# Kernel tuning notes

Measured on AMD Instinct MI355X. Metric: run time of the kernel, lower is better.

The kernel has to match this reference:

```python
import jax, jax.numpy as jnp
import numpy as np

N_Q = 8          # number of residual quantizer stages
N_CODES = 1024   # 2 ** (75 // N_q + 1)
D = 128
GAMMA = 0.99


def setup_inputs() -> dict:
    key = jax.random.key(0)
    k1, k2, k3, k4 = jax.random.split(key, 4)
    data_object = jax.random.normal(k1, (16, D, 2048), dtype=jnp.float32)
    weights = jax.random.normal(k2, (N_Q, N_CODES, D), dtype=jnp.float32)
    # EMA cluster-size buffer; scale so most codes are 'alive' (>= 2)
    N_i = jax.random.uniform(k3, (N_Q, N_CODES), dtype=jnp.float32) * 100.0
    m_i = jax.random.normal(k4, (N_Q, N_CODES, D), dtype=jnp.float32)
    return {"data_object": data_object, "weights": weights, "N_i": N_i, "m_i": m_i}


def reference(data_object, weights, N_i, m_i):
    b, d, s = data_object.shape
    y = jnp.transpose(data_object, (0, 2, 1))  # [b, s, D]
    residual = y
    cur_y = jnp.zeros_like(y)
    all_idx, new_Ni, new_mi, new_W = [], [], [], []
    key = jax.random.key(42)
    one_m_g = 1.0 - GAMMA
    for i in range(N_Q):
        W = weights[i]  # [N, D]
        # squared euclidean distances: ||y||^2 + ||W||^2 - 2 y.W^T  -> [b, s, N]
        dist = ((residual ** 2).sum(-1)[..., None]
                + (W ** 2).sum(-1)[None, None, :]
                - 2.0 * jnp.einsum('bsd,nd->bsn', residual, W))
        idx = jnp.argmin(dist, axis=-1)          # [b, s]
        Q = W[idx]                               # gather  [b, s, D]
        cur_y = cur_y + Q
        flat_idx = idx.reshape(-1)               # [b*s]
        flat_res = residual.reshape(-1, d)       # [b*s, D]
        # fused scatter-reduce replacing the torch per-code mask loop
        counts = jax.ops.segment_sum(jnp.ones(flat_idx.shape, jnp.float32),
                                     flat_idx, num_segments=N_CODES)
        sums = jax.ops.segment_sum(flat_res, flat_idx, num_segments=N_CODES)
        Ni_new = N_i[i] * GAMMA + counts * one_m_g
        mi_new = m_i[i] * GAMMA + sums * one_m_g
        w_new = mi_new / jnp.clip(Ni_new, 1e-8)[:, None]
        # dead-code replacement with random residual vectors
        dead = Ni_new < 2.0
        rid = jax.random.randint(jax.random.fold_in(key, i), (N_CODES,),
                                 0, flat_res.shape[0])
        w_new = jnp.where(dead[:, None], flat_res[rid], w_new)
        all_idx.append(idx)
        new_Ni.append(Ni_new)
        new_mi.append(mi_new)
        new_W.append(w_new)
        residual = residual - Q
    cur_y_t = jnp.transpose(cur_y, (0, 2, 1))  # [b, D, s]
    # straight-through estimator
    logits = data_object + jax.lax.stop_gradient(cur_y_t - data_object)
    commitment_loss = jnp.mean((jax.lax.stop_gradient(cur_y_t) - data_object) ** 2)
    indices = jnp.stack(all_idx, axis=0)  # [N_q, b, s]
    return (logits, commitment_loss, indices,
            jnp.stack(new_Ni), jnp.stack(new_mi), jnp.stack(new_W))
```

## Files before the change

### kernel.cpp

```cpp
#include <hip/hip_runtime.h>
#include <hip/hip_bf16.h>

#define NQ 8
#define NC 1024
#define DD 128
#define BB 16
#define SS 2048
#define RR (BB * SS)
#define GAMMA_F 0.99f
#define TAU 0.03f

typedef __attribute__((ext_vector_type(8))) short bf16x8;
typedef __attribute__((ext_vector_type(4))) float f32x4;

__device__ __forceinline__ ushort f2bf(float x) {
  __hip_bfloat16 b = __float2bfloat16(x);
  return *reinterpret_cast<ushort*>(&b);
}
__device__ __forceinline__ float bf2f(ushort u) {
  unsigned v = ((unsigned)u) << 16;
  return *reinterpret_cast<float*>(&v);
}

__global__ __launch_bounds__(256) void k_transpose_in(
    const float* __restrict__ data, float* __restrict__ res)
{
  __shared__ float tile[32][33];
  int b = blockIdx.z;
  int s0 = blockIdx.x << 5, d0 = blockIdx.y << 5;
  int tx = threadIdx.x, ty = threadIdx.y;
  #pragma unroll
  for (int r = 0; r < 32; r += 8)
    tile[ty + r][tx] = data[((size_t)b * DD + d0 + ty + r) * SS + s0 + tx];
  __syncthreads();
  #pragma unroll
  for (int r = 0; r < 32; r += 8)
    res[((size_t)b * SS + s0 + ty + r) * DD + d0 + tx] = tile[tx][ty + r];
}

__global__ void k_wsq(const float* __restrict__ W, float* __restrict__ wsq)
{
  int c = blockIdx.x * blockDim.x + threadIdx.x;
  if (c >= NQ * NC) return;
  const float4* p = reinterpret_cast<const float4*>(W + (size_t)c * DD);
  float s = 0.f;
  #pragma unroll 8
  for (int k = 0; k < DD / 4; ++k) {
    float4 v = p[k];
    s += v.x * v.x + v.y * v.y + v.z * v.z + v.w * v.w;
  }
  wsq[c] = s;
}

__global__ __launch_bounds__(256) void k_split(
    const float* __restrict__ src, ushort* __restrict__ dst)
{
  int i = blockIdx.x * 256 + threadIdx.x;
  int row = i >> 2, ks = i & 3;
  const float4* sp = reinterpret_cast<const float4*>(src + (size_t)row * DD + ks * 32);
  size_t gb = ((size_t)(row >> 4) * 8 + ks * 2) * 64 + (row & 15);
  #pragma unroll
  for (int kg = 0; kg < 4; ++kg) {
    float4 a = sp[kg * 2], b = sp[kg * 2 + 1];
    ushort4 h0, h1, l0, l1;
    h0.x = f2bf(a.x); l0.x = f2bf(a.x - bf2f(h0.x));
    h0.y = f2bf(a.y); l0.y = f2bf(a.y - bf2f(h0.y));
    h0.z = f2bf(a.z); l0.z = f2bf(a.z - bf2f(h0.z));
    h0.w = f2bf(a.w); l0.w = f2bf(a.w - bf2f(h0.w));
    h1.x = f2bf(b.x); l1.x = f2bf(b.x - bf2f(h1.x));
    h1.y = f2bf(b.y); l1.y = f2bf(b.y - bf2f(h1.y));
    h1.z = f2bf(b.z); l1.z = f2bf(b.z - bf2f(h1.z));
    h1.w = f2bf(b.w); l1.w = f2bf(b.w - bf2f(h1.w));
    ushort* ph = dst + (gb + kg * 16) * 8;
    *reinterpret_cast<ushort4*>(ph) = h0;
    *reinterpret_cast<ushort4*>(ph + 4) = h1;
    ushort* pl = ph + 64 * 8;
    *reinterpret_cast<ushort4*>(pl) = l0;
    *reinterpret_cast<ushort4*>(pl + 4) = l1;
  }
}

__global__ __launch_bounds__(256, 4) void k_argmin(
    float* __restrict__ res, ushort* __restrict__ res_hl,
    const ushort* __restrict__ w_hl, const float* __restrict__ W,
    const float* __restrict__ wsq,
    int* __restrict__ idxw, float* __restrict__ idxf,
    int* __restrict__ count, int* __restrict__ fb_count,
    int* __restrict__ fb_list, int stage)
{
  __shared__ float Lm1[4][16], Lm2[4][16];
  __shared__ int   Li1[4][16];
  __shared__ int   sidx[16];
  __shared__ int   sfb[16];

  const int t = threadIdx.x;
  const int l = t & 63;
  const int w = t >> 6;
  const int l15 = l & 15, kg = l >> 4;
  const int row0 = blockIdx.x * 16;
  const float* wsqs = wsq + stage * NC;
  const ushort* wb = w_hl + (size_t)stage * NC * 256;

  const size_t ab = (size_t)blockIdx.x * 8;
  bf16x8 ah[4], al[4];
  #pragma unroll
  for (int ks = 0; ks < 4; ++ks) {
    ah[ks] = *reinterpret_cast<const bf16x8*>(res_hl + ((ab + ks * 2) * 64 + l) * 8);
    al[ks] = *reinterpret_cast<const bf16x8*>(res_hl + ((ab + ks * 2 + 1) * 64 + l) * 8);
  }

  float m1[4], m2[4];
  int i1[4];
  #pragma unroll
  for (int rg = 0; rg < 4; ++rg) { m1[rg] = 3.4e38f; m2[rg] = 3.4e38f; i1[rg] = 0; }

  #pragma unroll 2
  for (int k = 0; k < 16; ++k) {
    int ct = w * 16 + k;
    size_t bb = (size_t)ct * 8;
    bf16x8 bh[4], bl[4];
    #pragma unroll
    for (int ks = 0; ks < 4; ++ks) {
      bh[ks] = *reinterpret_cast<const bf16x8*>(wb + ((bb + ks * 2) * 64 + l) * 8);
      bl[ks] = *reinterpret_cast<const bf16x8*>(wb + ((bb + ks * 2 + 1) * 64 + l) * 8);
    }
    f32x4 accP = {0.f, 0.f, 0.f, 0.f};
    f32x4 accQ = {0.f, 0.f, 0.f, 0.f};
    #pragma unroll
    for (int ks = 0; ks < 4; ++ks) {
      accP = __builtin_amdgcn_mfma_f32_16x16x32_bf16(ah[ks], bh[ks], accP, 0, 0, 0);
      accQ = __builtin_amdgcn_mfma_f32_16x16x32_bf16(al[ks], bh[ks], accQ, 0, 0, 0);
      accQ = __builtin_amdgcn_mfma_f32_16x16x32_bf16(ah[ks], bl[ks], accQ, 0, 0, 0);
    }
    int code = ct * 16 + l15;
    float sq = wsqs[code];
    #pragma unroll
    for (int rg = 0; rg < 4; ++rg) {
      float s = fmaf(-2.f, accP[rg] + accQ[rg], sq);
      if (s < m1[rg]) { m2[rg] = m1[rg]; m1[rg] = s; i1[rg] = code; }
      else if (s < m2[rg]) m2[rg] = s;
    }
  }

  #pragma unroll
  for (int mk = 1; mk <= 8; mk <<= 1) {
    #pragma unroll
    for (int rg = 0; rg < 4; ++rg) {
      float om1 = __shfl_xor(m1[rg], mk);
      int   oi  = __shfl_xor(i1[rg], mk);
      float om2 = __shfl_xor(m2[rg], mk);
      bool bwin = (om1 < m1[rg]) || (om1 == m1[rg] && oi < i1[rg]);
      float lose = bwin ? m1[rg] : om1;
      m2[rg] = fminf(fminf(m2[rg], om2), lose);
      if (bwin) { m1[rg] = om1; i1[rg] = oi; }
    }
  }
  if (l15 == 0) {
    #pragma unroll
    for (int rg = 0; rg < 4; ++rg) {
      Lm1[w][kg * 4 + rg] = m1[rg];
      Lm2[w][kg * 4 + rg] = m2[rg];
      Li1[w][kg * 4 + rg] = i1[rg];
    }
  }
  __syncthreads();

  if (t < 16) {
    float gm1 = Lm1[0][t], gm2 = Lm2[0][t];
    int gi = Li1[0][t];
    #pragma unroll
    for (int q = 1; q < 4; ++q) {
      float b1 = Lm1[q][t], b2 = Lm2[q][t];
      int bi = Li1[q][t];
      bool bwin = (b1 < gm1) || (b1 == gm1 && bi < gi);
      float lose = bwin ? gm1 : b1;
      gm2 = fminf(fminf(gm2, b2), lose);
      if (bwin) { gm1 = b1; gi = bi; }
    }
    int row = row0 + t;
    if (gm2 - gm1 > TAU) {
      idxw[row] = gi;
      idxf[row] = (float)gi;
      atomicAdd(&count[gi], 1);
      sidx[t] = gi; sfb[t] = 0;
    } else {
      int p = atomicAdd(fb_count, 1);
      fb_list[p] = row;
      sidx[t] = 0; sfb[t] = 1;
    }
  }
  __syncthreads();

  {
    int rloc = t >> 4, g = t & 15;
    if (!sfb[rloc]) {
      int row = row0 + rloc;
      int id = sidx[rloc];
      const float4* rp = reinterpret_cast<const float4*>(res + (size_t)row * DD + g * 8);
      const float4* qp = reinterpret_cast<const float4*>(W + ((size_t)stage * NC + id) * DD + g * 8);
      float4 r0 = rp[0], r1 = rp[1];
      float4 q0 = qp[0], q1 = qp[1];
      float4 o0, o1;
      o0.x = r0.x - q0.x; o0.y = r0.y - q0.y; o0.z = r0.z - q0.z; o0.w = r0.w - q0.w;
      o1.x = r1.x - q1.x; o1.y = r1.y - q1.y; o1.z = r1.z - q1.z; o1.w = r1.w - q1.w;
      float4* wp2 = reinterpret_cast<float4*>(res + (size_t)row * DD + g * 8);
      wp2[0] = o0; wp2[1] = o1;
      ushort4 h0, h1, l0, l1;
      h0.x = f2bf(o0.x); l0.x = f2bf(o0.x - bf2f(h0.x));
      h0.y = f2bf(o0.y); l0.y = f2bf(o0.y - bf2f(h0.y));
      h0.z = f2bf(o0.z); l0.z = f2bf(o0.z - bf2f(h0.z));
      h0.w = f2bf(o0.w); l0.w = f2bf(o0.w - bf2f(h0.w));
      h1.x = f2bf(o1.x); l1.x = f2bf(o1.x - bf2f(h1.x));
      h1.y = f2bf(o1.y); l1.y = f2bf(o1.y - bf2f(h1.y));
      h1.z = f2bf(o1.z); l1.z = f2bf(o1.z - bf2f(h1.z));
      h1.w = f2bf(o1.w); l1.w = f2bf(o1.w - bf2f(h1.w));
      int ks = g >> 2, kgg = g & 3;
      size_t gb = ((size_t)(row >> 4) * 8 + ks * 2) * 64 + kgg * 16 + (row & 15);
      ushort* ph = res_hl + gb * 8;
      *reinterpret_cast<ushort4*>(ph) = h0;
      *reinterpret_cast<ushort4*>(ph + 4) = h1;
      ushort* pl = ph + 64 * 8;
      *reinterpret_cast<ushort4*>(pl) = l0;
      *reinterpret_cast<ushort4*>(pl + 4) = l1;
    }
  }
}

__global__ __launch_bounds__(256) void k_fallback(
    float* __restrict__ res, ushort* __restrict__ res_hl,
    const float* __restrict__ W, const float* __restrict__ wsq,
    const int* __restrict__ fb_count, const int* __restrict__ fb_list,
    int* __restrict__ idxw, float* __restrict__ idxf,
    int* __restrict__ count, int stage)
{
  __shared__ float rr[128];
  __shared__ float sv[256];
  __shared__ int   si[256];
  int n = *fb_count;
  int t = threadIdx.x;
  for (int b = blockIdx.x; b < n; b += gridDim.x) {
    int row = fb_list[b];
    __syncthreads();
    if (t < 128) rr[t] = res[(size_t)row * DD + t];
    __syncthreads();
    float bm = 3.4e38f; int bi = 0;
    #pragma unroll
    for (int j = 0; j < 4; ++j) {
      int c = t + j * 256;
      const float4* wp = reinterpret_cast<const float4*>(W + ((size_t)stage * NC + c) * DD);
      float dot = 0.f;
      #pragma unroll 8
      for (int k = 0; k < 32; ++k) {
        float4 wv = wp[k];
        dot = fmaf(rr[4 * k + 0], wv.x, dot);
        dot = fmaf(rr[4 * k + 1], wv.y, dot);
        dot = fmaf(rr[4 * k + 2], wv.z, dot);
        dot = fmaf(rr[4 * k + 3], wv.w, dot);
      }
      float s = fmaf(-2.f, dot, wsq[stage * NC + c]);
      if (s < bm || (s == bm && c < bi)) { bm = s; bi = c; }
    }
    sv[t] = bm; si[t] = bi;
    __syncthreads();
    for (int sft = 128; sft > 0; sft >>= 1) {
      if (t < sft) {
        float ov = sv[t + sft]; int oi = si[t + sft];
        if (ov < sv[t] || (ov == sv[t] && oi < si[t])) { sv[t] = ov; si[t] = oi; }
      }
      __syncthreads();
    }
    int win = si[0];
    if (t == 0) {
      idxw[row] = win;
      idxf[row] = (float)win;
      atomicAdd(&count[win], 1);
    }
    if (t < 128) {
      float o = rr[t] - W[((size_t)stage * NC + win) * DD + t];
      res[(size_t)row * DD + t] = o;
      ushort hi = f2bf(o);
      ushort lo = f2bf(o - bf2f(hi));
      size_t g0 = ((size_t)(row >> 4) * 8 + (t >> 5) * 2) * 64 + ((t >> 3) & 3) * 16 + (row & 15);
      res_hl[g0 * 8 + (t & 7)] = hi;
      res_hl[(g0 + 64) * 8 + (t & 7)] = lo;
    }
  }
}

__global__ __launch_bounds__(1024) void k_scan(
    int* __restrict__ count, int* __restrict__ offs, int* __restrict__ pos)
{
  __shared__ int sc[1024];
  int t = threadIdx.x;
  sc[t] = count[t];
  __syncthreads();
  for (int off = 1; off < 1024; off <<= 1) {
    int v = (t >= off) ? sc[t - off] : 0;
    __syncthreads();
    sc[t] += v;
    __syncthreads();
  }
  offs[t + 1] = sc[t];
  if (t == 0) { offs[0] = 0; count[1024] = 0; }
  pos[t] = 0;
  count[t] = 0;
}

__global__ __launch_bounds__(256) void k_scatter(
    const int* __restrict__ idxw, const int* __restrict__ offs,
    int* __restrict__ pos, int* __restrict__ rows_sorted)
{
  int r = blockIdx.x * 256 + threadIdx.x;
  int c = idxw[r];
  int slot = offs[c] + atomicAdd(&pos[c], 1);
  rows_sorted[slot] = r;
}

__device__ __forceinline__ unsigned rotl32(unsigned v, int r) { return (v << r) | (v >> (32 - r)); }

__device__ void threefry2x32(unsigned ks0, unsigned ks1, unsigned x0, unsigned x1,
                             unsigned& o0, unsigned& o1)
{
  unsigned ks2 = ks0 ^ ks1 ^ 0x1BD11BDAu;
  x0 += ks0; x1 += ks1;
  x0 += x1; x1 = rotl32(x1, 13); x1 ^= x0;
  x0 += x1; x1 = rotl32(x1, 15); x1 ^= x0;
  x0 += x1; x1 = rotl32(x1, 26); x1 ^= x0;
  x0 += x1; x1 = rotl32(x1, 6);  x1 ^= x0;
  x0 += ks1; x1 += ks2 + 1u;
  x0 += x1; x1 = rotl32(x1, 17); x1 ^= x0;
  x0 += x1; x1 = rotl32(x1, 29); x1 ^= x0;
  x0 += x1; x1 = rotl32(x1, 16); x1 ^= x0;
  x0 += x1; x1 = rotl32(x1, 24); x1 ^= x0;
  x0 += ks2; x1 += ks0 + 2u;
  x0 += x1; x1 = rotl32(x1, 13); x1 ^= x0;
  x0 += x1; x1 = rotl32(x1, 15); x1 ^= x0;
  x0 += x1; x1 = rotl32(x1, 26); x1 ^= x0;
  x0 += x1; x1 = rotl32(x1, 6);  x1 ^= x0;
  x0 += ks0; x1 += ks1 + 3u;
  x0 += x1; x1 = rotl32(x1, 17); x1 ^= x0;
  x0 += x1; x1 = rotl32(x1, 29); x1 ^= x0;
  x0 += x1; x1 = rotl32(x1, 16); x1 ^= x0;
  x0 += x1; x1 = rotl32(x1, 24); x1 ^= x0;
  x0 += ks1; x1 += ks2 + 4u;
  x0 += x1; x1 = rotl32(x1, 13); x1 ^= x0;
  x0 += x1; x1 = rotl32(x1, 15); x1 ^= x0;
  x0 += x1; x1 = rotl32(x1, 26); x1 ^= x0;
  x0 += x1; x1 = rotl32(x1, 6);  x1 ^= x0;
  x0 += ks2; x1 += ks0 + 5u;
  o0 = x0; o1 = x1;
}

__global__ __launch_bounds__(1024) void k_finalize(
    const float* __restrict__ Ni_in, const float* __restrict__ mi_in,
    const int* __restrict__ offs, const int* __restrict__ rows_sorted,
    const float* __restrict__ res, const float* __restrict__ W,
    const int* __restrict__ idxw,
    float* __restrict__ outNi, float* __restrict__ outmi, float* __restrict__ outW,
    int stage)
{
  __shared__ float red[8][128];
  const float ONEMG = (float)(1.0 - 0.99);
  int c = blockIdx.x;
  int t = threadIdx.x;
  int d = t & 127;
  int jw = t >> 7;
  int base = offs[c];
  int cnt = offs[c + 1] - base;
  const int* rs = rows_sorted + base;

  float sum = 0.f;
  int j = jw;
  for (; j + 24 < cnt; j += 32) {
    int r0 = rs[j];
    int r1 = rs[j + 8];
    int r2 = rs[j + 16];
    int r3 = rs[j + 24];
    float v0 = res[(size_t)r0 * DD + d];
    float v1 = res[(size_t)r1 * DD + d];
    float v2 = res[(size_t)r2 * DD + d];
    float v3 = res[(size_t)r3 * DD + d];
    sum += v0 + v1 + v2 + v3;
  }
  for (; j < cnt; j += 8)
    sum += res[(size_t)rs[j] * DD + d];

  red[jw][d] = sum;
  __syncthreads();

  if (jw == 0) {
    float s8 = red[0][d] + red[1][d] + red[2][d] + red[3][d]
             + red[4][d] + red[5][d] + red[6][d] + red[7][d];
    float wc = W[((size_t)stage * NC + c) * DD + d];
    float sum_pre = fmaf((float)cnt, wc, s8);
    float ni = Ni_in[stage * NC + c] * GAMMA_F + (float)cnt * ONEMG;
    float mm = mi_in[((size_t)stage * NC + c) * DD + d] * GAMMA_F + sum_pre * ONEMG;
    float w = mm / fmaxf(ni, 1e-8f);
    if (ni < 2.0f) {
      unsigned K0, K1, a0, a1, b0, b1, o0, o1;
      threefry2x32(0u, 42u, 0u, (unsigned)stage, K0, K1);
      threefry2x32(K0, K1, 0u, 2u, a0, a1);
      threefry2x32(K0, K1, 1u, 3u, b0, b1);
      unsigned bits;
      if (c < 512) { threefry2x32(a1, b1, (unsigned)c, (unsigned)(c + 512), o0, o1); bits = o0; }
      else         { threefry2x32(a1, b1, (unsigned)(c - 512), (unsigned)c, o0, o1); bits = o1; }
      int rid = (int)(bits & 32767u);
      int idr = idxw[rid];
      w = res[(size_t)rid * DD + d] + W[((size_t)stage * NC + idr) * DD + d];
    }
    if (d == 0) outNi[stage * NC + c] = ni;
    size_t o = ((size_t)stage * NC + c) * DD + d;
    outmi[o] = mm;
    outW[o] = w;
  }
}

__global__ __launch_bounds__(256) void k_final(
    const float* __restrict__ data, const float* __restrict__ res,
    float* __restrict__ logits, float* __restrict__ partials)
{
  __shared__ float tile[32][33];
  __shared__ float wsum[4];
  int b = blockIdx.z, s0 = blockIdx.x << 5, d0 = blockIdx.y << 5;
  int tx = threadIdx.x, ty = threadIdx.y;
  #pragma unroll
  for (int r = 0; r < 32; r += 8)
    tile[ty + r][tx] = res[((size_t)b * SS + s0 + ty + r) * DD + d0 + tx];
  __syncthreads();
  float l = 0.f;
  #pragma unroll
  for (int r = 0; r < 32; r += 8) {
    int dv = d0 + ty + r, s = s0 + tx;
    size_t o = ((size_t)b * DD + dv) * SS + s;
    float rv = tile[tx][ty + r];
    logits[o] = data[o] - rv;
    l = fmaf(rv, rv, l);
  }
  #pragma unroll
  for (int m = 1; m < 64; m <<= 1) l += __shfl_xor(l, m);
  int lin = ty * 32 + tx;
  if ((lin & 63) == 0) wsum[lin >> 6] = l;
  __syncthreads();
  if (lin == 0) {
    int bl = (blockIdx.z * gridDim.y + blockIdx.y) * gridDim.x + blockIdx.x;
    partials[bl] = wsum[0] + wsum[1] + wsum[2] + wsum[3];
  }
}

__global__ __launch_bounds__(1024) void k_loss_reduce(
    const float* __restrict__ partials, float* __restrict__ loss)
{
  __shared__ float ws[16];
  int t = threadIdx.x;
  float s = partials[t] + partials[t + 1024] + partials[t + 2048] + partials[t + 3072];
  #pragma unroll
  for (int m = 1; m < 64; m <<= 1) s += __shfl_xor(s, m);
  if ((t & 63) == 0) ws[t >> 6] = s;
  __syncthreads();
  if (t < 16) {
    float v = ws[t];
    #pragma unroll
    for (int m = 1; m < 16; m <<= 1) v += __shfl_xor(v, m);
    if (t == 0) loss[0] = v * (1.0f / 4194304.0f);
  }
}

extern "C" void kernel_launch(void* const* d_in, const int* in_sizes, int n_in,
                              void* d_out, int out_size, void* d_ws, size_t ws_size,
                              hipStream_t stream)
{
  (void)in_sizes; (void)n_in; (void)out_size; (void)ws_size;
  const float* data = (const float*)d_in[0];
  const float* W    = (const float*)d_in[1];
  const float* Ni   = (const float*)d_in[2];
  const float* mi   = (const float*)d_in[3];

  float* out        = (float*)d_out;
  float* out_logits = out;
  float* out_loss   = out + (size_t)BB * DD * SS;
  float* out_idx    = out_loss + 1;
  float* out_Ni     = out_idx + (size_t)NQ * RR;
  float* out_mi     = out_Ni + (size_t)NQ * NC;
  float* out_W      = out_mi + (size_t)NQ * NC * DD;

  char* wp = (char*)d_ws;
  float*  resA        = (float*)wp;   wp += (size_t)RR * DD * 4;
  ushort* res_hl      = (ushort*)wp;  wp += (size_t)RR * DD * 4;
  ushort* w_hl        = (ushort*)wp;  wp += (size_t)NQ * NC * DD * 4;
  float*  wsq         = (float*)wp;   wp += (size_t)NQ * NC * 4;
  int*    idxw        = (int*)wp;     wp += (size_t)RR * 4;
  int*    fb_list     = (int*)wp;     wp += (size_t)RR * 4;
  int*    rows_sorted = (int*)wp;     wp += (size_t)RR * 4;
  int*    count       = (int*)wp;     wp += (size_t)1025 * 4;
  int*    fb_count    = count + 1024;
  int*    pos         = (int*)wp;     wp += (size_t)NC * 4;
  int*    offs        = (int*)wp;     wp += (size_t)(NC + 1) * 4;
  float*  partials    = (float*)wp;   wp += (size_t)4096 * 4;

  k_transpose_in<<<dim3(SS / 32, DD / 32, BB), dim3(32, 8), 0, stream>>>(data, resA);
  k_split<<<RR * 4 / 256, 256, 0, stream>>>(resA, res_hl);
  k_wsq<<<(NQ * NC + 255) / 256, 256, 0, stream>>>(W, wsq);
  k_split<<<NQ * NC * 4 / 256, 256, 0, stream>>>(W, w_hl);
  hipMemsetAsync(count, 0, 1025 * sizeof(int), stream);

  for (int i = 0; i < NQ; ++i) {
    k_argmin<<<RR / 16, 256, 0, stream>>>(resA, res_hl, w_hl, W, wsq, idxw,
                                          out_idx + (size_t)i * RR,
                                          count, fb_count, fb_list, i);
    k_fallback<<<512, 256, 0, stream>>>(resA, res_hl, W, wsq, fb_count, fb_list,
                                        idxw, out_idx + (size_t)i * RR, count, i);
    k_scan<<<1, 1024, 0, stream>>>(count, offs, pos);
    k_scatter<<<RR / 256, 256, 0, stream>>>(idxw, offs, pos, rows_sorted);
    k_finalize<<<NC, 1024, 0, stream>>>(Ni, mi, offs, rows_sorted, resA, W, idxw,
                                        out_Ni, out_mi, out_W, i);
  }

  k_final<<<dim3(SS / 32, DD / 32, BB), dim3(32, 8), 0, stream>>>(data, resA, out_logits, partials);
  k_loss_reduce<<<1, 1024, 0, stream>>>(partials, out_loss);
}
```

Before: 836.9 us.

## Process two code tiles per iteration and speculatively update residual for fallback rows

The argmin loop now handles two 16-code tiles per iteration with independent accumulators, reusing A fragments and exposing more MFMA parallelism. Launch bounds drop to 2 blocks per SM to allow the extra registers. Rows that are ambiguous now also write their approximate index and update the residual immediately, so the block takes no divergent branch. The fallback kernel reconstructs the original residual by adding back the speculatively subtracted codeword, which adds a load and a possible rounding difference.

```diff
diff --git a/kernel.cpp b/kernel.cpp
--- a/kernel.cpp
+++ b/kernel.cpp
@@ -80,7 +80,7 @@
   }
 }
 
-__global__ __launch_bounds__(256, 4) void k_argmin(
+__global__ __launch_bounds__(256, 2) void k_argmin(
     float* __restrict__ res, ushort* __restrict__ res_hl,
     const ushort* __restrict__ w_hl, const float* __restrict__ W,
     const float* __restrict__ wsq,
@@ -91,7 +91,6 @@
   __shared__ float Lm1[4][16], Lm2[4][16];
   __shared__ int   Li1[4][16];
   __shared__ int   sidx[16];
-  __shared__ int   sfb[16];
 
   const int t = threadIdx.x;
   const int l = t & 63;
@@ -114,31 +113,43 @@
   #pragma unroll
   for (int rg = 0; rg < 4; ++rg) { m1[rg] = 3.4e38f; m2[rg] = 3.4e38f; i1[rg] = 0; }
 
-  #pragma unroll 2
-  for (int k = 0; k < 16; ++k) {
-    int ct = w * 16 + k;
-    size_t bb = (size_t)ct * 8;
-    bf16x8 bh[4], bl[4];
+  #pragma unroll 1
+  for (int k8 = 0; k8 < 8; ++k8) {
+    const int ct0 = w * 16 + k8 * 2;
+    const size_t b0 = (size_t)ct0 * 8;
+    const size_t b1 = b0 + 8;
+    bf16x8 bh0[4], bl0[4], bh1[4], bl1[4];
     #pragma unroll
     for (int ks = 0; ks < 4; ++ks) {
-      bh[ks] = *reinterpret_cast<const bf16x8*>(wb + ((bb + ks * 2) * 64 + l) * 8);
-      bl[ks] = *reinterpret_cast<const bf16x8*>(wb + ((bb + ks * 2 + 1) * 64 + l) * 8);
-    }
-    f32x4 accP = {0.f, 0.f, 0.f, 0.f};
-    f32x4 accQ = {0.f, 0.f, 0.f, 0.f};
+      bh0[ks] = *reinterpret_cast<const bf16x8*>(wb + ((b0 + ks * 2) * 64 + l) * 8);
+      bl0[ks] = *reinterpret_cast<const bf16x8*>(wb + ((b0 + ks * 2 + 1) * 64 + l) * 8);
+      bh1[ks] = *reinterpret_cast<const bf16x8*>(wb + ((b1 + ks * 2) * 64 + l) * 8);
+      bl1[ks] = *reinterpret_cast<const bf16x8*>(wb + ((b1 + ks * 2 + 1) * 64 + l) * 8);
+    }
+    f32x4 p0 = {0.f, 0.f, 0.f, 0.f};
+    f32x4 q0 = {0.f, 0.f, 0.f, 0.f};
+    f32x4 p1 = {0.f, 0.f, 0.f, 0.f};
+    f32x4 q1 = {0.f, 0.f, 0.f, 0.f};
     #pragma unroll
     for (int ks = 0; ks < 4; ++ks) {
-      accP = __builtin_amdgcn_mfma_f32_16x16x32_bf16(ah[ks], bh[ks], accP, 0, 0, 0);
-      accQ = __builtin_amdgcn_mfma_f32_16x16x32_bf16(al[ks], bh[ks], accQ, 0, 0, 0);
-      accQ = __builtin_amdgcn_mfma_f32_16x16x32_bf16(ah[ks], bl[ks], accQ, 0, 0, 0);
-    }
-    int code = ct * 16 + l15;
-    float sq = wsqs[code];
+      p0 = __builtin_amdgcn_mfma_f32_16x16x32_bf16(ah[ks], bh0[ks], p0, 0, 0, 0);
+      p1 = __builtin_amdgcn_mfma_f32_16x16x32_bf16(ah[ks], bh1[ks], p1, 0, 0, 0);
+      q0 = __builtin_amdgcn_mfma_f32_16x16x32_bf16(al[ks], bh0[ks], q0, 0, 0, 0);
+      q1 = __builtin_amdgcn_mfma_f32_16x16x32_bf16(al[ks], bh1[ks], q1, 0, 0, 0);
+      q0 = __builtin_amdgcn_mfma_f32_16x16x32_bf16(ah[ks], bl0[ks], q0, 0, 0, 0);
+      q1 = __builtin_amdgcn_mfma_f32_16x16x32_bf16(ah[ks], bl1[ks], q1, 0, 0, 0);
+    }
+    int code0 = ct0 * 16 + l15;
+    float sq0 = wsqs[code0];
+    float sq1 = wsqs[code0 + 16];
     #pragma unroll
     for (int rg = 0; rg < 4; ++rg) {
-      float s = fmaf(-2.f, accP[rg] + accQ[rg], sq);
-      if (s < m1[rg]) { m2[rg] = m1[rg]; m1[rg] = s; i1[rg] = code; }
-      else if (s < m2[rg]) m2[rg] = s;
+      float s0 = fmaf(-2.f, p0[rg] + q0[rg], sq0);
+      if (s0 < m1[rg]) { m2[rg] = m1[rg]; m1[rg] = s0; i1[rg] = code0; }
+      else if (s0 < m2[rg]) m2[rg] = s0;
+      float s1 = fmaf(-2.f, p1[rg] + q1[rg], sq1);
+      if (s1 < m1[rg]) { m2[rg] = m1[rg]; m1[rg] = s1; i1[rg] = code0 + 16; }
+      else if (s1 < m2[rg]) m2[rg] = s1;
     }
   }
 
@@ -178,51 +189,48 @@
       if (bwin) { gm1 = b1; gi = bi; }
     }
     int row = row0 + t;
+    idxw[row] = gi;
+    idxf[row] = (float)gi;
+    sidx[t] = gi;
     if (gm2 - gm1 > TAU) {
-      idxw[row] = gi;
-      idxf[row] = (float)gi;
       atomicAdd(&count[gi], 1);
-      sidx[t] = gi; sfb[t] = 0;
     } else {
       int p = atomicAdd(fb_count, 1);
       fb_list[p] = row;
-      sidx[t] = 0; sfb[t] = 1;
     }
   }
   __syncthreads();
 
   {
     int rloc = t >> 4, g = t & 15;
-    if (!sfb[rloc]) {
-      int row = row0 + rloc;
-      int id = sidx[rloc];
-      const float4* rp = reinterpret_cast<const float4*>(res + (size_t)row * DD + g * 8);
-      const float4* qp = reinterpret_cast<const float4*>(W + ((size_t)stage * NC + id) * DD + g * 8);
-      float4 r0 = rp[0], r1 = rp[1];
-      float4 q0 = qp[0], q1 = qp[1];
-      float4 o0, o1;
-      o0.x = r0.x - q0.x; o0.y = r0.y - q0.y; o0.z = r0.z - q0.z; o0.w = r0.w - q0.w;
-      o1.x = r1.x - q1.x; o1.y = r1.y - q1.y; o1.z = r1.z - q1.z; o1.w = r1.w - q1.w;
-      float4* wp2 = reinterpret_cast<float4*>(res + (size_t)row * DD + g * 8);
-      wp2[0] = o0; wp2[1] = o1;
-      ushort4 h0, h1, l0, l1;
-      h0.x = f2bf(o0.x); l0.x = f2bf(o0.x - bf2f(h0.x));
-      h0.y = f2bf(o0.y); l0.y = f2bf(o0.y - bf2f(h0.y));
-      h0.z = f2bf(o0.z); l0.z = f2bf(o0.z - bf2f(h0.z));
-      h0.w = f2bf(o0.w); l0.w = f2bf(o0.w - bf2f(h0.w));
-      h1.x = f2bf(o1.x); l1.x = f2bf(o1.x - bf2f(h1.x));
-      h1.y = f2bf(o1.y); l1.y = f2bf(o1.y - bf2f(h1.y));
-      h1.z = f2bf(o1.z); l1.z = f2bf(o1.z - bf2f(h1.z));
-      h1.w = f2bf(o1.w); l1.w = f2bf(o1.w - bf2f(h1.w));
-      int ks = g >> 2, kgg = g & 3;
-      size_t gb = ((size_t)(row >> 4) * 8 + ks * 2) * 64 + kgg * 16 + (row & 15);
-      ushort* ph = res_hl + gb * 8;
-      *reinterpret_cast<ushort4*>(ph) = h0;
-      *reinterpret_cast<ushort4*>(ph + 4) = h1;
-      ushort* pl = ph + 64 * 8;
-      *reinterpret_cast<ushort4*>(pl) = l0;
-      *reinterpret_cast<ushort4*>(pl + 4) = l1;
-    }
+    int row = row0 + rloc;
+    int id = sidx[rloc];
+    const float4* rp = reinterpret_cast<const float4*>(res + (size_t)row * DD + g * 8);
+    const float4* qp = reinterpret_cast<const float4*>(W + ((size_t)stage * NC + id) * DD + g * 8);
+    float4 r0 = rp[0], r1 = rp[1];
+    float4 q0 = qp[0], q1 = qp[1];
+    float4 o0, o1;
+    o0.x = r0.x - q0.x; o0.y = r0.y - q0.y; o0.z = r0.z - q0.z; o0.w = r0.w - q0.w;
+    o1.x = r1.x - q1.x; o1.y = r1.y - q1.y; o1.z = r1.z - q1.z; o1.w = r1.w - q1.w;
+    float4* wp2 = reinterpret_cast<float4*>(res + (size_t)row * DD + g * 8);
+    wp2[0] = o0; wp2[1] = o1;
+    ushort4 h0, h1, l0, l1;
+    h0.x = f2bf(o0.x); l0.x = f2bf(o0.x - bf2f(h0.x));
+    h0.y = f2bf(o0.y); l0.y = f2bf(o0.y - bf2f(h0.y));
+    h0.z = f2bf(o0.z); l0.z = f2bf(o0.z - bf2f(h0.z));
+    h0.w = f2bf(o0.w); l0.w = f2bf(o0.w - bf2f(h0.w));
+    h1.x = f2bf(o1.x); l1.x = f2bf(o1.x - bf2f(h1.x));
+    h1.y = f2bf(o1.y); l1.y = f2bf(o1.y - bf2f(h1.y));
+    h1.z = f2bf(o1.z); l1.z = f2bf(o1.z - bf2f(h1.z));
+    h1.w = f2bf(o1.w); l1.w = f2bf(o1.w - bf2f(h1.w));
+    int ks = g >> 2, kgg = g & 3;
+    size_t gb = ((size_t)(row >> 4) * 8 + ks * 2) * 64 + kgg * 16 + (row & 15);
+    ushort* ph = res_hl + gb * 8;
+    *reinterpret_cast<ushort4*>(ph) = h0;
+    *reinterpret_cast<ushort4*>(ph + 4) = h1;
+    ushort* pl = ph + 64 * 8;
+    *reinterpret_cast<ushort4*>(pl) = l0;
+    *reinterpret_cast<ushort4*>(pl + 4) = l1;
   }
 }
 
@@ -240,8 +248,10 @@
   int t = threadIdx.x;
   for (int b = blockIdx.x; b < n; b += gridDim.x) {
     int row = fb_list[b];
+    int approx = idxw[row];
     __syncthreads();
-    if (t < 128) rr[t] = res[(size_t)row * DD + t];
+    if (t < 128)
+      rr[t] = res[(size_t)row * DD + t] + W[((size_t)stage * NC + approx) * DD + t];
     __syncthreads();
     float bm = 3.4e38f; int bi = 0;
     #pragma unroll
```

Measured after the change: 876.3 us. 1.05x slower.
